# Kernel optimization log

Measured on AMD Instinct MI355X. Metric: run time of the kernel, lower is better.

## Reference

```python
import jax, jax.numpy as jnp
import numpy as np

B, LQ, LK, H = 4, 256, 512, 256

def setup_inputs() -> dict:
    key = jax.random.key(0)
    ks = jax.random.split(key, 9)
    return {
        "query": jax.random.normal(ks[0], (B, LQ, H), dtype=jnp.float32),
        "key": jax.random.normal(ks[1], (B, LK, H), dtype=jnp.float32),
        "value": jax.random.normal(ks[2], (B, LK, H), dtype=jnp.float32),
        "mask": jax.random.randint(ks[3], (B, LK), 0, 2, dtype=jnp.int32),
        "Wq": jax.random.normal(ks[4], (H, H), dtype=jnp.float32) / np.sqrt(H),
        "bq": jnp.zeros((H,), dtype=jnp.float32),
        "Wk": jax.random.normal(ks[5], (H, H), dtype=jnp.float32) / np.sqrt(H),
        "bk": jnp.zeros((H,), dtype=jnp.float32),
        "v": jax.random.normal(ks[6], (H,), dtype=jnp.float32) / np.sqrt(H),
        "bv": jnp.zeros((), dtype=jnp.float32),
    }

def reference(query, key, value, mask, Wq, bq, Wk, bk, v, bv):
    # Linear projections: y = x @ W^T + b (torch nn.Linear convention)
    q = query @ Wq.T + bq            # [B, Lq, H]
    k = key @ Wk.T + bk              # [B, Lk, H]
    # Broadcast add -> tanh -> project to scalar with v
    s = jnp.tanh(q[:, :, None, :] + k[:, None, :, :])   # [B, Lq, Lk, H]
    scores = jnp.einsum('bqkh,h->bqk', s, v) + bv        # [B, Lq, Lk]
    scores = jnp.where(mask[:, None, :] == 0, -jnp.inf, scores)
    attn_weights = jax.nn.softmax(scores, axis=-1)       # [B, Lq, Lk]
    attn_output = jnp.einsum('bqk,bkh->bqh', attn_weights, value)
    return (attn_output, attn_weights)
```

## Files before the change

### kernel.cpp

```cpp
#include <hip/hip_runtime.h>
#include <math.h>

#define NB  4
#define NLQ 256
#define NLK 512
#define NH  256

#define SCALE_2LOG2E 2.885390081777927f
#define LOG2E        1.4426950408889634f

__global__ __launch_bounds__(256) void setup_kernel(
    const float* __restrict__ Wq, const float* __restrict__ Wk,
    const int* __restrict__ mask,
    float* __restrict__ Wtq, float* __restrict__ Wtk,
    int* __restrict__ act, int* __restrict__ nact)
{
    const int blk = blockIdx.x;
    const int t   = threadIdx.x;

    if (blk < 32) {
        __shared__ float ts[64][65];
        const int m    = blk >> 4;
        const int tile = blk & 15;
        const int h0 = (tile >> 2) * 64;
        const int c0 = (tile & 3) * 64;
        const float* W  = m ? Wk  : Wq;
        float*       Wt = m ? Wtk : Wtq;
        const int lr = t >> 4, lc = t & 15;
        #pragma unroll
        for (int i = 0; i < 4; ++i) {
            const int r = lr + 16 * i;
            const float4 d = *(const float4*)(W + (size_t)(h0 + r) * NH + c0 + lc * 4);
            ts[r][lc * 4 + 0] = d.x;
            ts[r][lc * 4 + 1] = d.y;
            ts[r][lc * 4 + 2] = d.z;
            ts[r][lc * 4 + 3] = d.w;
        }
        __syncthreads();
        #pragma unroll
        for (int i = 0; i < 4; ++i) {
            const int c = lr + 16 * i;
            float4 d;
            d.x = ts[lc * 4 + 0][c];
            d.y = ts[lc * 4 + 1][c];
            d.z = ts[lc * 4 + 2][c];
            d.w = ts[lc * 4 + 3][c];
            *(float4*)(Wt + (size_t)(c0 + c) * NH + h0 + lc * 4) = d;
        }
    } else if (blk < 32 + NB) {
        const int b = blk - 32;
        __shared__ int wcnt[8], wpre[9];
        const int lane = t & 63, wave = t >> 6;
        const int k1 = t, k2 = t + 256;
        const int m1 = mask[b * NLK + k1];
        const int m2 = mask[b * NLK + k2];
        const unsigned long long below = (1ULL << lane) - 1ULL;
        const unsigned long long bal1 = __ballot(m1 != 0);
        const unsigned long long bal2 = __ballot(m2 != 0);
        const int r1 = __popcll(bal1 & below);
        const int r2 = __popcll(bal2 & below);
        if (lane == 0) { wcnt[wave] = __popcll(bal1); wcnt[4 + wave] = __popcll(bal2); }
        __syncthreads();
        if (t == 0) {
            int s = 0;
            #pragma unroll
            for (int w = 0; w < 8; ++w) { wpre[w] = s; s += wcnt[w]; }
            wpre[8] = s;
        }
        __syncthreads();
        const int na = wpre[8];
        if (m1) act[b * NLK + wpre[wave]     + r1] = k1;
        if (m2) act[b * NLK + wpre[4 + wave] + r2] = k2;
        if (k1 >= na) act[b * NLK + k1] = 0;
        if (k2 >= na) act[b * NLK + k2] = 0;
        if (t == 0) nact[b] = na;
    }
}

__global__ __launch_bounds__(256) void prep_kernel(
    const float* __restrict__ query, const float* __restrict__ key,
    const float* __restrict__ Wtq, const float* __restrict__ bq,
    const float* __restrict__ Wtk, const float* __restrict__ bk,
    const int* __restrict__ act, const int* __restrict__ nact,
    float* __restrict__ qp, float* __restrict__ kp_ct)
{
    const int blk  = blockIdx.x;
    const int t    = threadIdx.x;
    const int wave = t >> 6;
    const int lane = t & 63;

    __shared__ float  xs[4][NH];
    __shared__ float4 ps[4][4][64];
    __shared__ int    ridx[4];

    const float *Wt, *bias;
    int b = 0, j0 = 0, r0 = 0, na = 0;
    const bool isq = (blk < NB * NLQ / 4);

    if (isq) {
        r0 = blk * 4;
        ((float4*)&xs[0][0])[t] = ((const float4*)(query + (size_t)r0 * NH))[t];
        Wt = Wtq; bias = bq;
    } else {
        b  = (blk - 256) >> 7;
        j0 = ((blk - 256) & 127) * 4;
        na = nact[b];
        if (j0 >= na) return;
        if (t < 4) ridx[t] = act[b * NLK + ((j0 + t < na) ? (j0 + t) : j0)];
        __syncthreads();
        const int r = t >> 6, c4 = t & 63;
        ((float4*)xs[r])[c4] =
            ((const float4*)(key + ((size_t)b * NLK + ridx[r]) * NH))[c4];
        Wt = Wtk; bias = bk;
    }
    __syncthreads();

    float4 acc[4];
    #pragma unroll
    for (int r = 0; r < 4; ++r) acc[r] = (float4){0.f, 0.f, 0.f, 0.f};

    const int cbase = wave * 64;
    #pragma unroll 4
    for (int cc = 0; cc < 64; ++cc) {
        const int c = cbase + cc;
        const float4 w = *(const float4*)(Wt + (size_t)c * NH + lane * 4);
        #pragma unroll
        for (int r = 0; r < 4; ++r) {
            const float xv = xs[r][c];
            acc[r].x = fmaf(xv, w.x, acc[r].x);
            acc[r].y = fmaf(xv, w.y, acc[r].y);
            acc[r].z = fmaf(xv, w.z, acc[r].z);
            acc[r].w = fmaf(xv, w.w, acc[r].w);
        }
    }
    #pragma unroll
    for (int r = 0; r < 4; ++r) ps[wave][r][lane] = acc[r];
    __syncthreads();

    const int r = wave, l = lane;
    const float4 p0 = ps[0][r][l], p1 = ps[1][r][l];
    const float4 p2 = ps[2][r][l], p3 = ps[3][r][l];
    const float4 bb = *(const float4*)(bias + l * 4);
    float4 o;
    o.x = (p0.x + p1.x + p2.x + p3.x + bb.x) * SCALE_2LOG2E;
    o.y = (p0.y + p1.y + p2.y + p3.y + bb.y) * SCALE_2LOG2E;
    o.z = (p0.z + p1.z + p2.z + p3.z + bb.z) * SCALE_2LOG2E;
    o.w = (p0.w + p1.w + p2.w + p3.w + bb.w) * SCALE_2LOG2E;
    o.x = __builtin_amdgcn_exp2f(o.x);
    o.y = __builtin_amdgcn_exp2f(o.y);
    o.z = __builtin_amdgcn_exp2f(o.z);
    o.w = __builtin_amdgcn_exp2f(o.w);

    if (isq) {
        *(float4*)(qp + (size_t)(r0 + r) * NH + l * 4) = o;
    } else if (j0 + r < na) {
        const int j = j0 + r;
        kp_ct[((size_t)b * NH + l * 4 + 0) * NLK + j] = o.x;
        kp_ct[((size_t)b * NH + l * 4 + 1) * NLK + j] = o.y;
        kp_ct[((size_t)b * NH + l * 4 + 2) * NLK + j] = o.z;
        kp_ct[((size_t)b * NH + l * 4 + 3) * NLK + j] = o.w;
    }
}

__global__ __launch_bounds__(512) void attn_kernel(
    const float* __restrict__ qp, const float* __restrict__ kp_ct,
    const float* __restrict__ value, const int* __restrict__ mask,
    const int* __restrict__ act, const int* __restrict__ nact,
    const float* __restrict__ vvec,
    float* __restrict__ out_o, float* __restrict__ out_w)
{
    __shared__ float sc0[NLK], sc1[NLK];
    __shared__ int   actl[NLK];
    __shared__ float eqs[2][NH];
    __shared__ float vvs[NH];
    __shared__ float4 buf4[1024];

    const int blk  = blockIdx.x;
    const int b    = blk >> 7;
    const int q0   = (blk & 127) * 2;
    const int t    = threadIdx.x;
    const int lane = t & 63;
    const int wave = t >> 6;

    const int na = nact[b];
    actl[t] = (t < na) ? act[b * NLK + t] : 0;
    if (t < NH) {
        eqs[0][t] = qp[(size_t)(b * NLQ + q0) * NH + t];
        eqs[1][t] = qp[(size_t)(b * NLQ + q0 + 1) * NH + t];
        vvs[t]    = vvec[t];
    }

    float* w0row = out_w + (size_t)(b * NLQ + q0) * NLK;
    float* w1row = w0row + NLK;
    if (!mask[b * NLK + t]) { w0row[t] = 0.f; w1row[t] = 0.f; }
    __syncthreads();

    const int cb = wave * 32;
    const float* kb  = kp_ct + ((size_t)b * NH + cb) * NLK;
    const float* eq0 = &eqs[0][cb];
    const float* eq1 = &eqs[1][cb];
    const float* vv  = &vvs[cb];

    float4 a0 = {0.f, 0.f, 0.f, 0.f}, a1 = {0.f, 0.f, 0.f, 0.f};
    #pragma unroll 4
    for (int c = 0; c < 32; ++c) {
        const float4 kx = *(const float4*)(kb + (size_t)c * NLK + 4 * lane);
        const float eqa = eq0[c];
        const float eqb = eq1[c];
        const float vh  = vv[c];
        a0.x = fmaf(vh, __builtin_amdgcn_rcpf(fmaf(eqa, kx.x, 1.f)), a0.x);
        a0.y = fmaf(vh, __builtin_amdgcn_rcpf(fmaf(eqa, kx.y, 1.f)), a0.y);
        a0.z = fmaf(vh, __builtin_amdgcn_rcpf(fmaf(eqa, kx.z, 1.f)), a0.z);
        a0.w = fmaf(vh, __builtin_amdgcn_rcpf(fmaf(eqa, kx.w, 1.f)), a0.w);
        a1.x = fmaf(vh, __builtin_amdgcn_rcpf(fmaf(eqb, kx.x, 1.f)), a1.x);
        a1.y = fmaf(vh, __builtin_amdgcn_rcpf(fmaf(eqb, kx.y, 1.f)), a1.y);
        a1.z = fmaf(vh, __builtin_amdgcn_rcpf(fmaf(eqb, kx.z, 1.f)), a1.z);
        a1.w = fmaf(vh, __builtin_amdgcn_rcpf(fmaf(eqb, kx.w, 1.f)), a1.w);
    }
    buf4[(0 * 8 + wave) * 64 + lane] = a0;
    buf4[(1 * 8 + wave) * 64 + lane] = a1;
    __syncthreads();
    {
        const int r = t >> 8, s = t & 255;
        const float* p = (const float*)buf4 + r * 2048;
        float sum = 0.f;
        #pragma unroll
        for (int o = 0; o < 8; ++o) sum += p[o * 256 + s];
        (r ? sc1 : sc0)[s] = (s < na) ? -2.f * sum : -INFINITY;
    }

    if (na > 256) {
        __syncthreads();
        float4 b0 = {0.f, 0.f, 0.f, 0.f}, b1 = {0.f, 0.f, 0.f, 0.f};
        const int s0 = 256 + 4 * lane;
        if (s0 < na) {
            #pragma unroll 4
            for (int c = 0; c < 32; ++c) {
                const float4 kx = *(const float4*)(kb + (size_t)c * NLK + s0);
                const float eqa = eq0[c];
                const float eqb = eq1[c];
                const float vh  = vv[c];
                b0.x = fmaf(vh, __builtin_amdgcn_rcpf(fmaf(eqa, kx.x, 1.f)), b0.x);
                b0.y = fmaf(vh, __builtin_amdgcn_rcpf(fmaf(eqa, kx.y, 1.f)), b0.y);
                b0.z = fmaf(vh, __builtin_amdgcn_rcpf(fmaf(eqa, kx.z, 1.f)), b0.z);
                b0.w = fmaf(vh, __builtin_amdgcn_rcpf(fmaf(eqa, kx.w, 1.f)), b0.w);
                b1.x = fmaf(vh, __builtin_amdgcn_rcpf(fmaf(eqb, kx.x, 1.f)), b1.x);
                b1.y = fmaf(vh, __builtin_amdgcn_rcpf(fmaf(eqb, kx.y, 1.f)), b1.y);
                b1.z = fmaf(vh, __builtin_amdgcn_rcpf(fmaf(eqb, kx.z, 1.f)), b1.z);
                b1.w = fmaf(vh, __builtin_amdgcn_rcpf(fmaf(eqb, kx.w, 1.f)), b1.w);
            }
        }
        buf4[(0 * 8 + wave) * 64 + lane] = b0;
        buf4[(1 * 8 + wave) * 64 + lane] = b1;
        __syncthreads();
        const int r = t >> 8, s = t & 255;
        const float* p = (const float*)buf4 + r * 2048;
        float sum = 0.f;
        #pragma unroll
        for (int o = 0; o < 8; ++o) sum += p[o * 256 + s];
        (r ? sc1 : sc0)[256 + s] = (256 + s < na) ? -2.f * sum : -INFINITY;
    } else {
        const int r = t >> 8, s = t & 255;
        (r ? sc1 : sc0)[256 + s] = -INFINITY;
    }
    __syncthreads();

    if (wave < 2) {
        float* row = wave ? sc1 : sc0;
        float vals[8];
        float m = -INFINITY;
        #pragma unroll
        for (int j8 = 0; j8 < 8; ++j8) {
            vals[j8] = row[lane + j8 * 64];
            m = fmaxf(m, vals[j8]);
        }
        #pragma unroll
        for (int s = 32; s >= 1; s >>= 1)
            m = fmaxf(m, __shfl_xor(m, s, 64));
        float sum = 0.0f;
        #pragma unroll
        for (int j8 = 0; j8 < 8; ++j8) {
            vals[j8] = __builtin_amdgcn_exp2f((vals[j8] - m) * LOG2E);
            sum += vals[j8];
        }
        #pragma unroll
        for (int s = 32; s >= 1; s >>= 1)
            sum += __shfl_xor(sum, s, 64);
        const float inv = __builtin_amdgcn_rcpf(sum);
        float* wout = out_w + (size_t)(b * NLQ + q0 + wave) * NLK;
        #pragma unroll
        for (int j8 = 0; j8 < 8; ++j8) {
            const int jj = lane + j8 * 64;
            const float w = vals[j8] * inv;
            row[jj] = w;
            if (jj < na) wout[actl[jj]] = w;
        }
    }
    __syncthreads();

    {
        const int c4 = lane * 4;
        const float* vb = value + (size_t)b * NLK * NH + c4;
        float4 o0 = {0.f, 0.f, 0.f, 0.f}, o1 = {0.f, 0.f, 0.f, 0.f};
        #pragma unroll 4
        for (int j = wave; j < na; j += 8) {
            const float w0 = sc0[j];
            const float w1 = sc1[j];
            const int   rj = actl[j];
            const float4 v4 = *(const float4*)(vb + (size_t)rj * NH);
            o0.x = fmaf(w0, v4.x, o0.x); o0.y = fmaf(w0, v4.y, o0.y);
            o0.z = fmaf(w0, v4.z, o0.z); o0.w = fmaf(w0, v4.w, o0.w);
            o1.x = fmaf(w1, v4.x, o1.x); o1.y = fmaf(w1, v4.y, o1.y);
            o1.z = fmaf(w1, v4.z, o1.z); o1.w = fmaf(w1, v4.w, o1.w);
        }
        buf4[t]       = o0;
        buf4[512 + t] = o1;
        __syncthreads();
        if (t < 128) {
            const int row = t >> 6;
            const int l   = t & 63;
            float4 o = buf4[row * 512 + l];
            #pragma unroll
            for (int w = 1; w < 8; ++w) {
                const float4 s = buf4[row * 512 + l + 64 * w];
                o.x += s.x; o.y += s.y; o.z += s.z; o.w += s.w;
            }
            *(float4*)(out_o + (size_t)(b * NLQ + q0 + row) * NH + l * 4) = o;
        }
    }
}

extern "C" void kernel_launch(void* const* d_in, const int* in_sizes, int n_in,
                              void* d_out, int out_size, void* d_ws, size_t ws_size,
                              hipStream_t stream) {
    const float* query = (const float*)d_in[0];
    const float* key   = (const float*)d_in[1];
    const float* value = (const float*)d_in[2];
    const int*   mask  = (const int*)  d_in[3];
    const float* Wq    = (const float*)d_in[4];
    const float* bq    = (const float*)d_in[5];
    const float* Wk    = (const float*)d_in[6];
    const float* bk    = (const float*)d_in[7];
    const float* v     = (const float*)d_in[8];

    float* out_o = (float*)d_out;
    float* out_w = out_o + NB * NLQ * NH;

    float* qp    = (float*)d_ws;
    float* kp_ct = qp + NB * NLQ * NH;
    int*   act   = (int*)(kp_ct + NB * NH * NLK);
    int*   nact  = act + NB * NLK;

    const size_t base = (size_t)(NB * NLQ * NH) + (size_t)(NB * NH * NLK)
                      + NB * NLK + NB;
    float* wtq;
    if (ws_size >= (base + 2 * NH * NH) * sizeof(float)) {
        wtq = (float*)d_ws + base;
    } else {
        wtq = out_w + (size_t)NB * NLQ * NLK - 2 * NH * NH;
    }
    float* wtk = wtq + NH * NH;

    setup_kernel<<<36, 256, 0, stream>>>(Wq, Wk, mask, wtq, wtk, act, nact);
    prep_kernel<<<NB * NLQ / 4 + NB * NLK / 4, 256, 0, stream>>>(
        query, key, wtq, bq, wtk, bk, act, nact, qp, kp_ct);
    attn_kernel<<<NB * NLQ / 2, 512, 0, stream>>>(
        qp, kp_ct, value, mask, act, nact, v, out_o, out_w);
}
```

Baseline: 112.1 us.

## Interleave batches across blocks and fuse both key halves into one score pass

Block indices in the projection and attention kernels now map batch to the low bits, so neighbouring blocks work on different batches. This is meant to balance work when the number of active keys differs per batch. The attention score loop now handles both 256-key halves in a single pass, with four accumulators and one reduction, replacing a second loop and extra barriers. In exchange the LDS reduction buffer doubles in size and register pressure rises, which may lower occupancy.

```diff
diff --git a/kernel.cpp b/kernel.cpp
--- a/kernel.cpp
+++ b/kernel.cpp
@@ -98,12 +98,14 @@
     const bool isq = (blk < NB * NLQ / 4);
 
     if (isq) {
-        r0 = blk * 4;
+        b  = blk & 3;
+        r0 = b * NLQ + (blk >> 2) * 4;
         ((float4*)&xs[0][0])[t] = ((const float4*)(query + (size_t)r0 * NH))[t];
         Wt = Wtq; bias = bq;
     } else {
-        b  = (blk - 256) >> 7;
-        j0 = ((blk - 256) & 127) * 4;
+        const int idx = blk - 256;
+        b  = idx & 3;
+        j0 = (idx >> 2) * 4;
         na = nact[b];
         if (j0 >= na) return;
         if (t < 4) ridx[t] = act[b * NLK + ((j0 + t < na) ? (j0 + t) : j0)];
@@ -173,11 +175,11 @@
     __shared__ int   actl[NLK];
     __shared__ float eqs[2][NH];
     __shared__ float vvs[NH];
-    __shared__ float4 buf4[1024];
+    __shared__ float4 buf4[2048];
 
     const int blk  = blockIdx.x;
-    const int b    = blk >> 7;
-    const int q0   = (blk & 127) * 2;
+    const int b    = blk & 3;
+    const int q0   = (blk >> 2) * 2;
     const int t    = threadIdx.x;
     const int lane = t & 63;
     const int wave = t >> 6;
@@ -202,66 +204,64 @@
     const float* vv  = &vvs[cb];
 
     float4 a0 = {0.f, 0.f, 0.f, 0.f}, a1 = {0.f, 0.f, 0.f, 0.f};
-    #pragma unroll 4
-    for (int c = 0; c < 32; ++c) {
-        const float4 kx = *(const float4*)(kb + (size_t)c * NLK + 4 * lane);
-        const float eqa = eq0[c];
-        const float eqb = eq1[c];
-        const float vh  = vv[c];
-        a0.x = fmaf(vh, __builtin_amdgcn_rcpf(fmaf(eqa, kx.x, 1.f)), a0.x);
-        a0.y = fmaf(vh, __builtin_amdgcn_rcpf(fmaf(eqa, kx.y, 1.f)), a0.y);
-        a0.z = fmaf(vh, __builtin_amdgcn_rcpf(fmaf(eqa, kx.z, 1.f)), a0.z);
-        a0.w = fmaf(vh, __builtin_amdgcn_rcpf(fmaf(eqa, kx.w, 1.f)), a0.w);
-        a1.x = fmaf(vh, __builtin_amdgcn_rcpf(fmaf(eqb, kx.x, 1.f)), a1.x);
-        a1.y = fmaf(vh, __builtin_amdgcn_rcpf(fmaf(eqb, kx.y, 1.f)), a1.y);
-        a1.z = fmaf(vh, __builtin_amdgcn_rcpf(fmaf(eqb, kx.z, 1.f)), a1.z);
-        a1.w = fmaf(vh, __builtin_amdgcn_rcpf(fmaf(eqb, kx.w, 1.f)), a1.w);
-    }
-    buf4[(0 * 8 + wave) * 64 + lane] = a0;
-    buf4[(1 * 8 + wave) * 64 + lane] = a1;
+    float4 a2 = {0.f, 0.f, 0.f, 0.f}, a3 = {0.f, 0.f, 0.f, 0.f};
+    if (na > 256) {
+        #pragma unroll 4
+        for (int c = 0; c < 32; ++c) {
+            const float4 k1 = *(const float4*)(kb + (size_t)c * NLK + 4 * lane);
+            const float4 k2 = *(const float4*)(kb + (size_t)c * NLK + 256 + 4 * lane);
+            const float eqa = eq0[c];
+            const float eqb = eq1[c];
+            const float vh  = vv[c];
+            a0.x = fmaf(vh, __builtin_amdgcn_rcpf(fmaf(eqa, k1.x, 1.f)), a0.x);
+            a0.y = fmaf(vh, __builtin_amdgcn_rcpf(fmaf(eqa, k1.y, 1.f)), a0.y);
+            a0.z = fmaf(vh, __builtin_amdgcn_rcpf(fmaf(eqa, k1.z, 1.f)), a0.z);
+            a0.w = fmaf(vh, __builtin_amdgcn_rcpf(fmaf(eqa, k1.w, 1.f)), a0.w);
+            a1.x = fmaf(vh, __builtin_amdgcn_rcpf(fmaf(eqb, k1.x, 1.f)), a1.x);
+            a1.y = fmaf(vh, __builtin_amdgcn_rcpf(fmaf(eqb, k1.y, 1.f)), a1.y);
+            a1.z = fmaf(vh, __builtin_amdgcn_rcpf(fmaf(eqb, k1.z, 1.f)), a1.z);
+            a1.w = fmaf(vh, __builtin_amdgcn_rcpf(fmaf(eqb, k1.w, 1.f)), a1.w);
+            a2.x = fmaf(vh, __builtin_amdgcn_rcpf(fmaf(eqa, k2.x, 1.f)), a2.x);
+            a2.y = fmaf(vh, __builtin_amdgcn_rcpf(fmaf(eqa, k2.y, 1.f)), a2.y);
+            a2.z = fmaf(vh, __builtin_amdgcn_rcpf(fmaf(eqa, k2.z, 1.f)), a2.z);
+            a2.w = fmaf(vh, __builtin_amdgcn_rcpf(fmaf(eqa, k2.w, 1.f)), a2.w);
+            a3.x = fmaf(vh, __builtin_amdgcn_rcpf(fmaf(eqb, k2.x, 1.f)), a3.x);
+            a3.y = fmaf(vh, __builtin_amdgcn_rcpf(fmaf(eqb, k2.y, 1.f)), a3.y);
+            a3.z = fmaf(vh, __builtin_amdgcn_rcpf(fmaf(eqb, k2.z, 1.f)), a3.z);
+            a3.w = fmaf(vh, __builtin_amdgcn_rcpf(fmaf(eqb, k2.w, 1.f)), a3.w);
+        }
+    } else {
+        #pragma unroll 4
+        for (int c = 0; c < 32; ++c) {
+            const float4 k1 = *(const float4*)(kb + (size_t)c * NLK + 4 * lane);
+            const float eqa = eq0[c];
+            const float eqb = eq1[c];
+            const float vh  = vv[c];
+            a0.x = fmaf(vh, __builtin_amdgcn_rcpf(fmaf(eqa, k1.x, 1.f)), a0.x);
+            a0.y = fmaf(vh, __builtin_amdgcn_rcpf(fmaf(eqa, k1.y, 1.f)), a0.y);
+            a0.z = fmaf(vh, __builtin_amdgcn_rcpf(fmaf(eqa, k1.z, 1.f)), a0.z);
+            a0.w = fmaf(vh, __builtin_amdgcn_rcpf(fmaf(eqa, k1.w, 1.f)), a0.w);
+            a1.x = fmaf(vh, __builtin_amdgcn_rcpf(fmaf(eqb, k1.x, 1.f)), a1.x);
+            a1.y = fmaf(vh, __builtin_amdgcn_rcpf(fmaf(eqb, k1.y, 1.f)), a1.y);
+            a1.z = fmaf(vh, __builtin_amdgcn_rcpf(fmaf(eqb, k1.z, 1.f)), a1.z);
+            a1.w = fmaf(vh, __builtin_amdgcn_rcpf(fmaf(eqb, k1.w, 1.f)), a1.w);
+        }
+    }
+    buf4[(0 * 8 + wave) * 128 + lane]      = a0;
+    buf4[(0 * 8 + wave) * 128 + 64 + lane] = a2;
+    buf4[(1 * 8 + wave) * 128 + lane]      = a1;
+    buf4[(1 * 8 + wave) * 128 + 64 + lane] = a3;
     __syncthreads();
     {
-        const int r = t >> 8, s = t & 255;
-        const float* p = (const float*)buf4 + r * 2048;
-        float sum = 0.f;
-        #pragma unroll
-        for (int o = 0; o < 8; ++o) sum += p[o * 256 + s];
-        (r ? sc1 : sc0)[s] = (s < na) ? -2.f * sum : -INFINITY;
-    }
-
-    if (na > 256) {
-        __syncthreads();
-        float4 b0 = {0.f, 0.f, 0.f, 0.f}, b1 = {0.f, 0.f, 0.f, 0.f};
-        const int s0 = 256 + 4 * lane;
-        if (s0 < na) {
-            #pragma unroll 4
-            for (int c = 0; c < 32; ++c) {
-                const float4 kx = *(const float4*)(kb + (size_t)c * NLK + s0);
-                const float eqa = eq0[c];
-                const float eqb = eq1[c];
-                const float vh  = vv[c];
-                b0.x = fmaf(vh, __builtin_amdgcn_rcpf(fmaf(eqa, kx.x, 1.f)), b0.x);
-                b0.y = fmaf(vh, __builtin_amdgcn_rcpf(fmaf(eqa, kx.y, 1.f)), b0.y);
-                b0.z = fmaf(vh, __builtin_amdgcn_rcpf(fmaf(eqa, kx.z, 1.f)), b0.z);
-                b0.w = fmaf(vh, __builtin_amdgcn_rcpf(fmaf(eqa, kx.w, 1.f)), b0.w);
-                b1.x = fmaf(vh, __builtin_amdgcn_rcpf(fmaf(eqb, kx.x, 1.f)), b1.x);
-                b1.y = fmaf(vh, __builtin_amdgcn_rcpf(fmaf(eqb, kx.y, 1.f)), b1.y);
-                b1.z = fmaf(vh, __builtin_amdgcn_rcpf(fmaf(eqb, kx.z, 1.f)), b1.z);
-                b1.w = fmaf(vh, __builtin_amdgcn_rcpf(fmaf(eqb, kx.w, 1.f)), b1.w);
-            }
-        }
-        buf4[(0 * 8 + wave) * 64 + lane] = b0;
-        buf4[(1 * 8 + wave) * 64 + lane] = b1;
-        __syncthreads();
-        const int r = t >> 8, s = t & 255;
-        const float* p = (const float*)buf4 + r * 2048;
-        float sum = 0.f;
-        #pragma unroll
-        for (int o = 0; o < 8; ++o) sum += p[o * 256 + s];
-        (r ? sc1 : sc0)[256 + s] = (256 + s < na) ? -2.f * sum : -INFINITY;
-    } else {
-        const int r = t >> 8, s = t & 255;
-        (r ? sc1 : sc0)[256 + s] = -INFINITY;
+        const float* pf = (const float*)buf4;
+        float sA = 0.f, sB = 0.f;
+        #pragma unroll
+        for (int o = 0; o < 8; ++o) {
+            sA += pf[o * 512 + t];
+            sB += pf[(8 + o) * 512 + t];
+        }
+        sc0[t] = (t < na) ? -2.f * sA : -INFINITY;
+        sc1[t] = (t < na) ? -2.f * sB : -INFINITY;
     }
     __syncthreads();
 
```

After: 106.8 us. -4.7%, faster.
